# Kernel tuning notes

Measured on AMD Instinct MI355X. Metric: run time of the kernel, lower is better.

## Reference

```python
import jax, jax.numpy as jnp
import numpy as np

N_SRC = 50000
N_DST = 50000
N_EDGES = 1_600_000
D_IN = 128
D_OUT = 128
NUM_HEADS = 8
SCALE = float((D_OUT // NUM_HEADS) ** 0.5)


def setup_inputs() -> dict:
    key = jax.random.key(0)
    ks = jax.random.split(key, 10)
    s = 1.0 / np.sqrt(D_IN)
    return {
        "src_feat": jax.random.normal(ks[0], (N_SRC, D_IN), dtype=jnp.float32),
        "dst_feat": jax.random.normal(ks[1], (N_DST, D_OUT), dtype=jnp.float32),
        "src_idx": jax.random.randint(ks[2], (N_EDGES,), 0, N_SRC, dtype=jnp.int64),
        "dst_idx": jax.random.randint(ks[3], (N_EDGES,), 0, N_DST, dtype=jnp.int64),
        "Wq": jax.random.normal(ks[4], (D_OUT, D_OUT), dtype=jnp.float32) * s,
        "bq": jnp.zeros((D_OUT,), dtype=jnp.float32),
        "Wk": jax.random.normal(ks[5], (D_OUT, D_IN), dtype=jnp.float32) * s,
        "bk": jnp.zeros((D_OUT,), dtype=jnp.float32),
        "Wv": jax.random.normal(ks[6], (D_OUT, D_IN), dtype=jnp.float32) * s,
        "bv": jnp.zeros((D_OUT,), dtype=jnp.float32),
    }


def reference(src_feat, dst_feat, src_idx, dst_idx, Wq, bq, Wk, bk, Wv, bv):
    # Node-level projections (torch Linear: x @ W.T + b)
    Q = dst_feat @ Wq.T + bq            # [N_dst, D_OUT]
    K = src_feat @ Wk.T + bk            # [N_src, D_OUT]
    V = src_feat @ Wv.T + bv            # [N_src, D_OUT]

    # Edge-wise full-dim dot-product score (heads only affect the scale)
    score = jnp.sum(Q[dst_idx] * K[src_idx], axis=-1) / SCALE  # [E]

    # Segment softmax over incoming edges of each destination node
    m = jax.ops.segment_max(score, dst_idx, num_segments=N_DST)   # [N_dst]
    e = jnp.exp(score - m[dst_idx])                               # [E]
    denom = jax.ops.segment_sum(e, dst_idx, num_segments=N_DST)   # [N_dst]
    attn = e / denom[dst_idx]                                     # [E]

    # Weighted V scatter-sum to destination nodes
    out = jax.ops.segment_sum(attn[:, None] * V[src_idx], dst_idx,
                              num_segments=N_DST)                 # [N_dst, D_OUT]
    return out
```

## Files before the change

kernel.cpp:

```cpp
#include <hip/hip_runtime.h>
#include <hip/hip_bf16.h>


#define D 128
#define E1 4096
#define BCAP 10240
#define LOG2E 1.44269504088896340736f

typedef __attribute__((ext_vector_type(8))) short bf16x8;
typedef __attribute__((ext_vector_type(4))) float f32x4;
typedef __attribute__((ext_vector_type(4))) int v4i;
typedef __attribute__((ext_vector_type(4))) unsigned v4u;

static __device__ __forceinline__ unsigned short f2bf(float f) {
  unsigned u = __float_as_uint(f);
  u += 0x7fff + ((u >> 16) & 1);
  return (unsigned short)(u >> 16);
}
static __device__ __forceinline__ float bfl(unsigned u) {
  return __uint_as_float(u << 16);
}
static __device__ __forceinline__ float bfh(unsigned u) {
  return __uint_as_float(u & 0xffff0000u);
}

template <int CTRL>
static __device__ __forceinline__ float dpp_add(float x) {
  int y = __builtin_amdgcn_update_dpp(0, __float_as_int(x), CTRL, 0xF, 0xF, false);
  return x + __int_as_float(y);
}

static __device__ __forceinline__ float dot8(const float4& qa, const float4& qb,
                                             const v4u k0, const v4u k1) {
  return (qa.x * bfl(k0.x) + qa.y * bfh(k0.x) + qa.z * bfl(k0.y) +
          qa.w * bfh(k0.y)) +
         (qb.x * bfl(k1.x) + qb.y * bfh(k1.x) + qb.z * bfl(k1.y) +
          qb.w * bfh(k1.y));
}


static __device__ __forceinline__ void cvt_w_body(
    int bx, const float* __restrict__ Wq, const float* __restrict__ Wk,
    const float* __restrict__ Wv, unsigned short* __restrict__ oq,
    unsigned short* __restrict__ ok, unsigned short* __restrict__ ov, int n) {
  int i = bx * 256 + threadIdx.x;
  if (i < n) {
    oq[i] = f2bf(Wq[i]);
    ok[i] = f2bf(Wk[i]);
    ov[i] = f2bf(Wv[i]);
  }
}

static __device__ void bin1_body(
    int bx, int* h, int* basebuf, int* cur, const int* __restrict__ src_idx,
    const int* __restrict__ dst_idx, int* __restrict__ bins,
    int* __restrict__ bcount, int n) {
  const int tid = threadIdx.x;
  const int e0 = bx * E1;
  int dv[16], sv[16];
#pragma unroll
  for (int i = 0; i < 4; ++i) {
    int e = e0 + i * 1024 + tid * 4;
    if (e + 3 < n) {
      v4i d4 = __builtin_nontemporal_load((const v4i*)(dst_idx + e));
      v4i s4 = __builtin_nontemporal_load((const v4i*)(src_idx + e));
      dv[4 * i + 0] = d4.x; dv[4 * i + 1] = d4.y;
      dv[4 * i + 2] = d4.z; dv[4 * i + 3] = d4.w;
      sv[4 * i + 0] = s4.x; sv[4 * i + 1] = s4.y;
      sv[4 * i + 2] = s4.z; sv[4 * i + 3] = s4.w;
    } else {
      for (int k = 0; k < 4; ++k) {
        int ee = e + k;
        dv[4 * i + k] = (ee < n) ? dst_idx[ee] : -1;
        sv[4 * i + k] = (ee < n) ? src_idx[ee] : 0;
      }
    }
  }
  h[tid] = 0;
  __syncthreads();
#pragma unroll
  for (int i = 0; i < 16; ++i)
    if (dv[i] >= 0) atomicAdd(&h[dv[i] >> 8], 1);
  __syncthreads();
  const int c = h[tid];
  if (c > 0) basebuf[tid] = tid * BCAP + atomicAdd(&bcount[tid], c);
  cur[tid] = 0;
  __syncthreads();
#pragma unroll
  for (int i = 0; i < 16; ++i) {
    if (dv[i] >= 0) {
      const int b = dv[i] >> 8;
      const int r = atomicAdd(&cur[b], 1);
      const int off = basebuf[b] + r;
      if (off < (b + 1) * BCAP)
        bins[off] = sv[i] | ((dv[i] & 255) << 17);
    }
  }
}

static __device__ void bin2_body(
    int b, int* smem, const int* __restrict__ bins,
    const int* __restrict__ bcount, int* __restrict__ csr,
    int* __restrict__ rowptr, int n_dst, int n_edges) {
  int* h = smem;
  int* ofs = smem + 256;
  int* cur = smem + 512;
  int* red = smem + 768;
  const int tid = threadIdx.x;
  red[tid] = (tid < b) ? min(bcount[tid], BCAP) : 0;
  __syncthreads();
  for (int off = 128; off > 0; off >>= 1) {
    if (tid < off) red[tid] += red[tid + off];
    __syncthreads();
  }
  const int gbase = red[0];
  const int cnt = min(bcount[b], BCAP);
  h[tid] = 0;
  __syncthreads();
  const int* bb = bins + b * BCAP;
  for (int i = tid; i < cnt; i += 256) atomicAdd(&h[(bb[i] >> 17) & 255], 1);
  __syncthreads();
  const int myh = h[tid];
  red[tid] = myh;
  __syncthreads();
  for (int off = 1; off < 256; off <<= 1) {
    int t = (tid >= off) ? red[tid - off] : 0;
    __syncthreads();
    red[tid] += t;
    __syncthreads();
  }
  ofs[tid] = red[tid] - myh;
  cur[tid] = 0;
  const int d = b * 256 + tid;
  if (d < n_dst) rowptr[d] = gbase + ofs[tid];
  if (b == 0 && tid == 0) rowptr[n_dst] = n_edges;
  __syncthreads();
  for (int i = tid; i < cnt; i += 256) {
    const int p = bb[i];
    const int j = (p >> 17) & 255;
    const int r = atomicAdd(&cur[j], 1);
    csr[gbase + ofs[j] + r] = p & 0x1ffff;
  }
}

static __device__ void gemm_q_body(
    int bx, const float* __restrict__ X, const unsigned short* __restrict__ Wb,
    const float* __restrict__ bias, float* __restrict__ out, int N) {
  const int lane = threadIdx.x & 63;
  const int l15 = lane & 15, quad = lane >> 4;
  const int row0 = bx * 64 + (threadIdx.x >> 6) * 16;

  f32x4 acc[8];
#pragma unroll
  for (int t = 0; t < 8; ++t) acc[t] = (f32x4){0.f, 0.f, 0.f, 0.f};

  int ar = row0 + l15;
  if (ar >= N) ar = N - 1;
  const float* ap = X + (size_t)ar * D + quad * 8;

#pragma unroll
  for (int kc = 0; kc < 4; ++kc) {
    float4 a0 = *(const float4*)(ap + kc * 32);
    float4 a1 = *(const float4*)(ap + kc * 32 + 4);
    bf16x8 a;
    a[0] = f2bf(a0.x); a[1] = f2bf(a0.y); a[2] = f2bf(a0.z); a[3] = f2bf(a0.w);
    a[4] = f2bf(a1.x); a[5] = f2bf(a1.y); a[6] = f2bf(a1.z); a[7] = f2bf(a1.w);
#pragma unroll
    for (int t = 0; t < 8; ++t) {
      bf16x8 b =
          *(const bf16x8*)(Wb + (size_t)(t * 16 + l15) * D + kc * 32 + quad * 8);
      acc[t] = __builtin_amdgcn_mfma_f32_16x16x32_bf16(a, b, acc[t], 0, 0, 0);
    }
  }
#pragma unroll
  for (int t = 0; t < 8; ++t) {
    const int c = t * 16 + l15;
    const float bc = bias[c];
#pragma unroll
    for (int r = 0; r < 4; ++r) {
      const int row = row0 + quad * 4 + r;
      if (row < N) out[(size_t)row * D + c] = acc[t][r] + bc;
    }
  }
}

static __device__ void gemm_kv_body(
    int bx, unsigned short (*stage)[256], const float* __restrict__ X,
    const unsigned short* __restrict__ Wk, const float* __restrict__ bk,
    const unsigned short* __restrict__ Wv, const float* __restrict__ bv,
    unsigned short* __restrict__ KV, int N) {
  const int tid = threadIdx.x;
  const int lane = tid & 63;
  const int l15 = lane & 15, quad = lane >> 4;
  const int wave = tid >> 6;
  const int row0 = bx * 64 + wave * 16;

  f32x4 accK[8], accV[8];
#pragma unroll
  for (int t = 0; t < 8; ++t) {
    accK[t] = (f32x4){0.f, 0.f, 0.f, 0.f};
    accV[t] = (f32x4){0.f, 0.f, 0.f, 0.f};
  }

  int ar = row0 + l15;
  if (ar >= N) ar = N - 1;
  const float* ap = X + (size_t)ar * D + quad * 8;

#pragma unroll
  for (int kc = 0; kc < 4; ++kc) {
    float4 a0 = *(const float4*)(ap + kc * 32);
    float4 a1 = *(const float4*)(ap + kc * 32 + 4);
    bf16x8 a;
    a[0] = f2bf(a0.x); a[1] = f2bf(a0.y); a[2] = f2bf(a0.z); a[3] = f2bf(a0.w);
    a[4] = f2bf(a1.x); a[5] = f2bf(a1.y); a[6] = f2bf(a1.z); a[7] = f2bf(a1.w);
#pragma unroll
    for (int t = 0; t < 8; ++t) {
      const size_t boff = (size_t)(t * 16 + l15) * D + kc * 32 + quad * 8;
      bf16x8 b0 = *(const bf16x8*)(Wk + boff);
      bf16x8 b1 = *(const bf16x8*)(Wv + boff);
      accK[t] = __builtin_amdgcn_mfma_f32_16x16x32_bf16(a, b0, accK[t], 0, 0, 0);
      accV[t] = __builtin_amdgcn_mfma_f32_16x16x32_bf16(a, b1, accV[t], 0, 0, 0);
    }
  }
#pragma unroll
  for (int t = 0; t < 8; ++t) {
    const int c = t * 16 + l15;
    const float bkc = bk[c], bvc = bv[c];
    const int ki = ((c >> 2) << 3) + (c & 3);
#pragma unroll
    for (int r = 0; r < 4; ++r) {
      const int lr = wave * 16 + quad * 4 + r;
      stage[lr][ki] = f2bf(accK[t][r] + bkc);
      stage[lr][ki + 4] = f2bf(accV[t][r] + bvc);
    }
  }
  __syncthreads();
  const int row_base = bx * 64;
#pragma unroll
  for (int i = 0; i < 8; ++i) {
    int idx = i * 256 + tid;
    int lr = idx >> 5;
    int c8 = (idx & 31) << 3;
    int grow = row_base + lr;
    if (grow < N)
      *(f32x4*)(KV + (size_t)grow * 256 + c8) = *(const f32x4*)&stage[lr][c8];
  }
}


__global__ __launch_bounds__(256) void front_kernel(
    const float* __restrict__ Wq, const float* __restrict__ Wk,
    const float* __restrict__ Wv, unsigned short* __restrict__ oq,
    unsigned short* __restrict__ ok, unsigned short* __restrict__ ov, int nw,
    const int* __restrict__ src_idx, const int* __restrict__ dst_idx,
    int* __restrict__ bins, int* __restrict__ bcount, int n_edges, int gcvt) {
  __shared__ int sh[768];
  const int b = blockIdx.x;
  if (b < gcvt) {
    cvt_w_body(b, Wq, Wk, Wv, oq, ok, ov, nw);
  } else {
    bin1_body(b - gcvt, sh, sh + 256, sh + 512, src_idx, dst_idx, bins, bcount,
              n_edges);
  }
}

__global__ __launch_bounds__(256) void mid_kernel(
    const float* __restrict__ dst_feat, const unsigned short* __restrict__ Wqb,
    const float* __restrict__ bq, float* __restrict__ Q, int n_dst,
    const float* __restrict__ src_feat, const unsigned short* __restrict__ Wkb,
    const float* __restrict__ bk, const unsigned short* __restrict__ Wvb,
    const float* __restrict__ bv, unsigned short* __restrict__ KV, int n_src,
    const int* __restrict__ bins, const int* __restrict__ bcount,
    int* __restrict__ csr, int* __restrict__ rowptr, int n_edges, int nbk,
    int gq) {
  __shared__ unsigned short stage[64][256];
  const int b = blockIdx.x;
  if (b < nbk) {
    bin2_body(b, (int*)stage, bins, bcount, csr, rowptr, n_dst, n_edges);
  } else if (b < nbk + gq) {
    gemm_q_body(b - nbk, dst_feat, Wqb, bq, Q, n_dst);
  } else {
    gemm_kv_body(b - nbk - gq, stage, src_feat, Wkb, bk, Wvb, bv, KV, n_src);
  }
}

__global__ __launch_bounds__(256) void fused_agg_kernel(
    const float* __restrict__ Q, const unsigned short* __restrict__ KV,
    const int* __restrict__ csr, const int* __restrict__ rowptr,
    float* __restrict__ out, int n_dst) {
  const int lane = threadIdx.x & 63;
  const int g = lane >> 4;
  const int gl = lane & 15;
  const int stride = gridDim.x * 4;
  const float qs = 0.25f * LOG2E;

  for (int dd = blockIdx.x * 4 + (threadIdx.x >> 6); dd < n_dst; dd += stride) {
    const int d = __builtin_amdgcn_readfirstlane(dd);
    const int start = __builtin_amdgcn_readfirstlane(rowptr[d]);
    const int n = __builtin_amdgcn_readfirstlane(rowptr[d + 1]) - start;

    float4 q0 = *(const float4*)(Q + (size_t)d * D + 4 * gl);
    float4 q1 = *(const float4*)(Q + (size_t)d * D + 64 + 4 * gl);
    q0.x *= qs; q0.y *= qs; q0.z *= qs; q0.w *= qs;
    q1.x *= qs; q1.y *= qs; q1.z *= qs; q1.w *= qs;

    f32x4 acc0 = (f32x4){0.f, 0.f, 0.f, 0.f};
    f32x4 acc1 = (f32x4){0.f, 0.f, 0.f, 0.f};
    float den = 0.f;
    const int* cp = csr + start;

    for (int base = 0; base < n; base += 64) {
      const int il = base + lane;
      const int iv = __builtin_nontemporal_load(cp + ((il < n) ? il : (n - 1)));
      const int m = min(64, n - base);
      for (int j = 0; j < m; j += 16) {
        const int s0 = __shfl(iv, j + g, 64);
        const int s1 = __shfl(iv, j + 4 + g, 64);
        const int s2 = __shfl(iv, j + 8 + g, 64);
        const int s3 = __shfl(iv, j + 12 + g, 64);
        const unsigned short* r0 = KV + (size_t)s0 * 256 + gl * 8;
        const unsigned short* r1 = KV + (size_t)s1 * 256 + gl * 8;
        const unsigned short* r2 = KV + (size_t)s2 * 256 + gl * 8;
        const unsigned short* r3 = KV + (size_t)s3 * 256 + gl * 8;
        const v4u a0 = *(const v4u*)(r0);
        const v4u a1 = *(const v4u*)(r0 + 128);
        const v4u b0 = *(const v4u*)(r1);
        const v4u b1 = *(const v4u*)(r1 + 128);
        const v4u c0 = *(const v4u*)(r2);
        const v4u c1 = *(const v4u*)(r2 + 128);
        const v4u e0 = *(const v4u*)(r3);
        const v4u e1 = *(const v4u*)(r3 + 128);

        float p0 = dot8(q0, q1, a0, a1);
        float p1 = dot8(q0, q1, b0, b1);
        float p2 = dot8(q0, q1, c0, c1);
        float p3 = dot8(q0, q1, e0, e1);

        p0 = dpp_add<0xB1>(p0);  p1 = dpp_add<0xB1>(p1);
        p2 = dpp_add<0xB1>(p2);  p3 = dpp_add<0xB1>(p3);
        p0 = dpp_add<0x4E>(p0);  p1 = dpp_add<0x4E>(p1);
        p2 = dpp_add<0x4E>(p2);  p3 = dpp_add<0x4E>(p3);
        p0 = dpp_add<0x141>(p0); p1 = dpp_add<0x141>(p1);
        p2 = dpp_add<0x141>(p2); p3 = dpp_add<0x141>(p3);
        p0 = dpp_add<0x140>(p0); p1 = dpp_add<0x140>(p1);
        p2 = dpp_add<0x140>(p2); p3 = dpp_add<0x140>(p3);

        const float w0 = (j + g < m)      ? exp2f(p0) : 0.f;
        const float w1 = (j + 4 + g < m)  ? exp2f(p1) : 0.f;
        const float w2 = (j + 8 + g < m)  ? exp2f(p2) : 0.f;
        const float w3 = (j + 12 + g < m) ? exp2f(p3) : 0.f;

        acc0[0] += w0 * bfl(a0.z) + w1 * bfl(b0.z) + w2 * bfl(c0.z) + w3 * bfl(e0.z);
        acc0[1] += w0 * bfh(a0.z) + w1 * bfh(b0.z) + w2 * bfh(c0.z) + w3 * bfh(e0.z);
        acc0[2] += w0 * bfl(a0.w) + w1 * bfl(b0.w) + w2 * bfl(c0.w) + w3 * bfl(e0.w);
        acc0[3] += w0 * bfh(a0.w) + w1 * bfh(b0.w) + w2 * bfh(c0.w) + w3 * bfh(e0.w);
        acc1[0] += w0 * bfl(a1.z) + w1 * bfl(b1.z) + w2 * bfl(c1.z) + w3 * bfl(e1.z);
        acc1[1] += w0 * bfh(a1.z) + w1 * bfh(b1.z) + w2 * bfh(c1.z) + w3 * bfh(e1.z);
        acc1[2] += w0 * bfl(a1.w) + w1 * bfl(b1.w) + w2 * bfl(c1.w) + w3 * bfl(e1.w);
        acc1[3] += w0 * bfh(a1.w) + w1 * bfh(b1.w) + w2 * bfh(c1.w) + w3 * bfh(e1.w);
        den += (w0 + w1) + (w2 + w3);
      }
    }

#pragma unroll
    for (int msk = 16; msk <= 32; msk <<= 1) {
      acc0[0] += __shfl_xor(acc0[0], msk, 64);
      acc0[1] += __shfl_xor(acc0[1], msk, 64);
      acc0[2] += __shfl_xor(acc0[2], msk, 64);
      acc0[3] += __shfl_xor(acc0[3], msk, 64);
      acc1[0] += __shfl_xor(acc1[0], msk, 64);
      acc1[1] += __shfl_xor(acc1[1], msk, 64);
      acc1[2] += __shfl_xor(acc1[2], msk, 64);
      acc1[3] += __shfl_xor(acc1[3], msk, 64);
      den += __shfl_xor(den, msk, 64);
    }

    if (lane < 16) {
      const float r = (n > 0) ? 1.0f / den : 0.f;
      f32x4 o0 = (f32x4){acc0[0] * r, acc0[1] * r, acc0[2] * r, acc0[3] * r};
      f32x4 o1 = (f32x4){acc1[0] * r, acc1[1] * r, acc1[2] * r, acc1[3] * r};
      __builtin_nontemporal_store(o0, (f32x4*)(out + (size_t)d * D + 4 * gl));
      __builtin_nontemporal_store(o1,
                                  (f32x4*)(out + (size_t)d * D + 64 + 4 * gl));
    }
  }
}

extern "C" void kernel_launch(void* const* d_in, const int* in_sizes, int n_in,
                              void* d_out, int out_size, void* d_ws,
                              size_t ws_size, hipStream_t stream) {
  const float* src_feat = (const float*)d_in[0];
  const float* dst_feat = (const float*)d_in[1];
  const int* src_idx = (const int*)d_in[2];
  const int* dst_idx = (const int*)d_in[3];
  const float* Wq = (const float*)d_in[4];
  const float* bq = (const float*)d_in[5];
  const float* Wk = (const float*)d_in[6];
  const float* bk = (const float*)d_in[7];
  const float* Wv = (const float*)d_in[8];
  const float* bv = (const float*)d_in[9];

  const int n_src = in_sizes[0] / D;
  const int n_dst = in_sizes[1] / D;
  const int n_edges = in_sizes[2];
  const int nbk = (n_dst + 255) >> 8;

  float* out = (float*)d_out;

  float* Q = (float*)d_ws;
  unsigned short* KV = (unsigned short*)(Q + (size_t)n_dst * D);
  unsigned short* Wqb = KV + (size_t)n_src * 256;
  unsigned short* Wkb = Wqb + D * D;
  unsigned short* Wvb = Wkb + D * D;
  int* bcount = (int*)(Wvb + D * D);
  int* rowptr = bcount + 256;
  int* csr = rowptr + (n_dst + 1);
  int* bins = csr + n_edges;

  (void)hipMemsetAsync(bcount, 0, 256 * sizeof(int), stream);

  dim3 blk(256);
  const int gcvt = (D * D + 255) / 256;
  const int g1 = (n_edges + E1 - 1) / E1;
  const int gq = (n_dst + 63) / 64;
  const int gkv = (n_src + 63) / 64;

  front_kernel<<<dim3(gcvt + g1), blk, 0, stream>>>(
      Wq, Wk, Wv, Wqb, Wkb, Wvb, D * D, src_idx, dst_idx, bins, bcount,
      n_edges, gcvt);

  mid_kernel<<<dim3(nbk + gq + gkv), blk, 0, stream>>>(
      dst_feat, Wqb, bq, Q, n_dst, src_feat, Wkb, bk, Wvb, bv, KV, n_src, bins,
      bcount, csr, rowptr, n_edges, nbk, gq);

  int gfa = (n_dst + 3) / 4;
  if (gfa > 2048) gfa = 2048;
  fused_agg_kernel<<<dim3(gfa), blk, 0, stream>>>(Q, KV, csr, rowptr, out,
                                                  n_dst);
}
```

Measured before the change: 291.0 us.

## Inline weight bf16 conversion into GEMMs and split aggregation into three launches

Removes the separate weight-conversion blocks and their workspace buffers, so the GEMMs now load fp32 weights and convert them to bf16 in registers. This drops a dependency stage but adds conversion work inside every GEMM tile. The aggregation kernel no longer uses a grid-stride loop and launches one block per four destinations, split across three identical kernels with offset indices. The extra launches add overhead, and any benefit from the split is unclear.

```diff
diff --git a/kernel.cpp b/kernel.cpp
--- a/kernel.cpp
+++ b/kernel.cpp
@@ -38,17 +38,14 @@
           qb.w * bfh(k1.y));
 }
 
-
-static __device__ __forceinline__ void cvt_w_body(
-    int bx, const float* __restrict__ Wq, const float* __restrict__ Wk,
-    const float* __restrict__ Wv, unsigned short* __restrict__ oq,
-    unsigned short* __restrict__ ok, unsigned short* __restrict__ ov, int n) {
-  int i = bx * 256 + threadIdx.x;
-  if (i < n) {
-    oq[i] = f2bf(Wq[i]);
-    ok[i] = f2bf(Wk[i]);
-    ov[i] = f2bf(Wv[i]);
-  }
+static __device__ __forceinline__ bf16x8 ldw(const float* __restrict__ W,
+                                             size_t off) {
+  float4 w0 = *(const float4*)(W + off);
+  float4 w1 = *(const float4*)(W + off + 4);
+  bf16x8 b;
+  b[0] = f2bf(w0.x); b[1] = f2bf(w0.y); b[2] = f2bf(w0.z); b[3] = f2bf(w0.w);
+  b[4] = f2bf(w1.x); b[5] = f2bf(w1.y); b[6] = f2bf(w1.z); b[7] = f2bf(w1.w);
+  return b;
 }
 
 static __device__ void bin1_body(
@@ -144,7 +141,7 @@
 }
 
 static __device__ void gemm_q_body(
-    int bx, const float* __restrict__ X, const unsigned short* __restrict__ Wb,
+    int bx, const float* __restrict__ X, const float* __restrict__ Wf,
     const float* __restrict__ bias, float* __restrict__ out, int N) {
   const int lane = threadIdx.x & 63;
   const int l15 = lane & 15, quad = lane >> 4;
@@ -167,8 +164,7 @@
     a[4] = f2bf(a1.x); a[5] = f2bf(a1.y); a[6] = f2bf(a1.z); a[7] = f2bf(a1.w);
 #pragma unroll
     for (int t = 0; t < 8; ++t) {
-      bf16x8 b =
-          *(const bf16x8*)(Wb + (size_t)(t * 16 + l15) * D + kc * 32 + quad * 8);
+      bf16x8 b = ldw(Wf, (size_t)(t * 16 + l15) * D + kc * 32 + quad * 8);
       acc[t] = __builtin_amdgcn_mfma_f32_16x16x32_bf16(a, b, acc[t], 0, 0, 0);
     }
   }
@@ -186,8 +182,8 @@
 
 static __device__ void gemm_kv_body(
     int bx, unsigned short (*stage)[256], const float* __restrict__ X,
-    const unsigned short* __restrict__ Wk, const float* __restrict__ bk,
-    const unsigned short* __restrict__ Wv, const float* __restrict__ bv,
+    const float* __restrict__ Wkf, const float* __restrict__ bk,
+    const float* __restrict__ Wvf, const float* __restrict__ bv,
     unsigned short* __restrict__ KV, int N) {
   const int tid = threadIdx.x;
   const int lane = tid & 63;
@@ -216,8 +212,8 @@
 #pragma unroll
     for (int t = 0; t < 8; ++t) {
       const size_t boff = (size_t)(t * 16 + l15) * D + kc * 32 + quad * 8;
-      bf16x8 b0 = *(const bf16x8*)(Wk + boff);
-      bf16x8 b1 = *(const bf16x8*)(Wv + boff);
+      bf16x8 b0 = ldw(Wkf, boff);
+      bf16x8 b1 = ldw(Wvf, boff);
       accK[t] = __builtin_amdgcn_mfma_f32_16x16x32_bf16(a, b0, accK[t], 0, 0, 0);
       accV[t] = __builtin_amdgcn_mfma_f32_16x16x32_bf16(a, b1, accV[t], 0, 0, 0);
     }
@@ -247,28 +243,120 @@
   }
 }
 
+static __device__ void fused_body(
+    int v, const float* __restrict__ Q, const unsigned short* __restrict__ KV,
+    const int* __restrict__ csr, const int* __restrict__ rowptr,
+    float* __restrict__ out, int n_dst) {
+  const int lane = threadIdx.x & 63;
+  const int g = lane >> 4;
+  const int gl = lane & 15;
+  int d = v * 4 + (threadIdx.x >> 6);
+  if (d >= n_dst) return;
+  d = __builtin_amdgcn_readfirstlane(d);
+  const int start = __builtin_amdgcn_readfirstlane(rowptr[d]);
+  const int n = __builtin_amdgcn_readfirstlane(rowptr[d + 1]) - start;
+
+  const float qs = 0.25f * LOG2E;
+  float4 q0 = *(const float4*)(Q + (size_t)d * D + 4 * gl);
+  float4 q1 = *(const float4*)(Q + (size_t)d * D + 64 + 4 * gl);
+  q0.x *= qs; q0.y *= qs; q0.z *= qs; q0.w *= qs;
+  q1.x *= qs; q1.y *= qs; q1.z *= qs; q1.w *= qs;
+
+  f32x4 acc0 = (f32x4){0.f, 0.f, 0.f, 0.f};
+  f32x4 acc1 = (f32x4){0.f, 0.f, 0.f, 0.f};
+  float den = 0.f;
+  const int* cp = csr + start;
+
+  for (int base = 0; base < n; base += 64) {
+    const int il = base + lane;
+    const int iv = __builtin_nontemporal_load(cp + ((il < n) ? il : (n - 1)));
+    const int m = min(64, n - base);
+    for (int j = 0; j < m; j += 16) {
+      const int s0 = __shfl(iv, j + g, 64);
+      const int s1 = __shfl(iv, j + 4 + g, 64);
+      const int s2 = __shfl(iv, j + 8 + g, 64);
+      const int s3 = __shfl(iv, j + 12 + g, 64);
+      const unsigned short* r0 = KV + (size_t)s0 * 256 + gl * 8;
+      const unsigned short* r1 = KV + (size_t)s1 * 256 + gl * 8;
+      const unsigned short* r2 = KV + (size_t)s2 * 256 + gl * 8;
+      const unsigned short* r3 = KV + (size_t)s3 * 256 + gl * 8;
+      const v4u a0 = *(const v4u*)(r0);
+      const v4u a1 = *(const v4u*)(r0 + 128);
+      const v4u b0 = *(const v4u*)(r1);
+      const v4u b1 = *(const v4u*)(r1 + 128);
+      const v4u c0 = *(const v4u*)(r2);
+      const v4u c1 = *(const v4u*)(r2 + 128);
+      const v4u e0 = *(const v4u*)(r3);
+      const v4u e1 = *(const v4u*)(r3 + 128);
+
+      float p0 = dot8(q0, q1, a0, a1);
+      float p1 = dot8(q0, q1, b0, b1);
+      float p2 = dot8(q0, q1, c0, c1);
+      float p3 = dot8(q0, q1, e0, e1);
+
+      p0 = dpp_add<0xB1>(p0);  p1 = dpp_add<0xB1>(p1);
+      p2 = dpp_add<0xB1>(p2);  p3 = dpp_add<0xB1>(p3);
+      p0 = dpp_add<0x4E>(p0);  p1 = dpp_add<0x4E>(p1);
+      p2 = dpp_add<0x4E>(p2);  p3 = dpp_add<0x4E>(p3);
+      p0 = dpp_add<0x141>(p0); p1 = dpp_add<0x141>(p1);
+      p2 = dpp_add<0x141>(p2); p3 = dpp_add<0x141>(p3);
+      p0 = dpp_add<0x140>(p0); p1 = dpp_add<0x140>(p1);
+      p2 = dpp_add<0x140>(p2); p3 = dpp_add<0x140>(p3);
+
+      const float w0 = (j + g < m)      ? exp2f(p0) : 0.f;
+      const float w1 = (j + 4 + g < m)  ? exp2f(p1) : 0.f;
+      const float w2 = (j + 8 + g < m)  ? exp2f(p2) : 0.f;
+      const float w3 = (j + 12 + g < m) ? exp2f(p3) : 0.f;
+
+      acc0[0] += w0 * bfl(a0.z) + w1 * bfl(b0.z) + w2 * bfl(c0.z) + w3 * bfl(e0.z);
+      acc0[1] += w0 * bfh(a0.z) + w1 * bfh(b0.z) + w2 * bfh(c0.z) + w3 * bfh(e0.z);
+      acc0[2] += w0 * bfl(a0.w) + w1 * bfl(b0.w) + w2 * bfl(c0.w) + w3 * bfl(e0.w);
+      acc0[3] += w0 * bfh(a0.w) + w1 * bfh(b0.w) + w2 * bfh(c0.w) + w3 * bfh(e0.w);
+      acc1[0] += w0 * bfl(a1.z) + w1 * bfl(b1.z) + w2 * bfl(c1.z) + w3 * bfl(e1.z);
+      acc1[1] += w0 * bfh(a1.z) + w1 * bfh(b1.z) + w2 * bfh(c1.z) + w3 * bfh(e1.z);
+      acc1[2] += w0 * bfl(a1.w) + w1 * bfl(b1.w) + w2 * bfl(c1.w) + w3 * bfl(e1.w);
+      acc1[3] += w0 * bfh(a1.w) + w1 * bfh(b1.w) + w2 * bfh(c1.w) + w3 * bfh(e1.w);
+      den += (w0 + w1) + (w2 + w3);
+    }
+  }
+
+#pragma unroll
+  for (int msk = 16; msk <= 32; msk <<= 1) {
+    acc0[0] += __shfl_xor(acc0[0], msk, 64);
+    acc0[1] += __shfl_xor(acc0[1], msk, 64);
+    acc0[2] += __shfl_xor(acc0[2], msk, 64);
+    acc0[3] += __shfl_xor(acc0[3], msk, 64);
+    acc1[0] += __shfl_xor(acc1[0], msk, 64);
+    acc1[1] += __shfl_xor(acc1[1], msk, 64);
+    acc1[2] += __shfl_xor(acc1[2], msk, 64);
+    acc1[3] += __shfl_xor(acc1[3], msk, 64);
+    den += __shfl_xor(den, msk, 64);
+  }
+
+  if (lane < 16) {
+    const float r = (n > 0) ? 1.0f / den : 0.f;
+    f32x4 o0 = (f32x4){acc0[0] * r, acc0[1] * r, acc0[2] * r, acc0[3] * r};
+    f32x4 o1 = (f32x4){acc1[0] * r, acc1[1] * r, acc1[2] * r, acc1[3] * r};
+    __builtin_nontemporal_store(o0, (f32x4*)(out + (size_t)d * D + 4 * gl));
+    __builtin_nontemporal_store(o1,
+                                (f32x4*)(out + (size_t)d * D + 64 + 4 * gl));
+  }
+}
+
 
 __global__ __launch_bounds__(256) void front_kernel(
-    const float* __restrict__ Wq, const float* __restrict__ Wk,
-    const float* __restrict__ Wv, unsigned short* __restrict__ oq,
-    unsigned short* __restrict__ ok, unsigned short* __restrict__ ov, int nw,
     const int* __restrict__ src_idx, const int* __restrict__ dst_idx,
-    int* __restrict__ bins, int* __restrict__ bcount, int n_edges, int gcvt) {
+    int* __restrict__ bins, int* __restrict__ bcount, int n_edges) {
   __shared__ int sh[768];
-  const int b = blockIdx.x;
-  if (b < gcvt) {
-    cvt_w_body(b, Wq, Wk, Wv, oq, ok, ov, nw);
-  } else {
-    bin1_body(b - gcvt, sh, sh + 256, sh + 512, src_idx, dst_idx, bins, bcount,
-              n_edges);
-  }
+  bin1_body(blockIdx.x, sh, sh + 256, sh + 512, src_idx, dst_idx, bins, bcount,
+            n_edges);
 }
 
 __global__ __launch_bounds__(256) void mid_kernel(
-    const float* __restrict__ dst_feat, const unsigned short* __restrict__ Wqb,
+    const float* __restrict__ dst_feat, const float* __restrict__ Wq,
     const float* __restrict__ bq, float* __restrict__ Q, int n_dst,
-    const float* __restrict__ src_feat, const unsigned short* __restrict__ Wkb,
-    const float* __restrict__ bk, const unsigned short* __restrict__ Wvb,
+    const float* __restrict__ src_feat, const float* __restrict__ Wk,
+    const float* __restrict__ bk, const float* __restrict__ Wv,
     const float* __restrict__ bv, unsigned short* __restrict__ KV, int n_src,
     const int* __restrict__ bins, const int* __restrict__ bcount,
     int* __restrict__ csr, int* __restrict__ rowptr, int n_edges, int nbk,
@@ -278,112 +366,29 @@
   if (b < nbk) {
     bin2_body(b, (int*)stage, bins, bcount, csr, rowptr, n_dst, n_edges);
   } else if (b < nbk + gq) {
-    gemm_q_body(b - nbk, dst_feat, Wqb, bq, Q, n_dst);
+    gemm_q_body(b - nbk, dst_feat, Wq, bq, Q, n_dst);
   } else {
-    gemm_kv_body(b - nbk - gq, stage, src_feat, Wkb, bk, Wvb, bv, KV, n_src);
-  }
-}
-
-__global__ __launch_bounds__(256) void fused_agg_kernel(
+    gemm_kv_body(b - nbk - gq, stage, src_feat, Wk, bk, Wv, bv, KV, n_src);
+  }
+}
+
+__global__ __launch_bounds__(256) void fused_agg_k0(
     const float* __restrict__ Q, const unsigned short* __restrict__ KV,
     const int* __restrict__ csr, const int* __restrict__ rowptr,
-    float* __restrict__ out, int n_dst) {
-  const int lane = threadIdx.x & 63;
-  const int g = lane >> 4;
-  const int gl = lane & 15;
-  const int stride = gridDim.x * 4;
-  const float qs = 0.25f * LOG2E;
-
-  for (int dd = blockIdx.x * 4 + (threadIdx.x >> 6); dd < n_dst; dd += stride) {
-    const int d = __builtin_amdgcn_readfirstlane(dd);
-    const int start = __builtin_amdgcn_readfirstlane(rowptr[d]);
-    const int n = __builtin_amdgcn_readfirstlane(rowptr[d + 1]) - start;
-
-    float4 q0 = *(const float4*)(Q + (size_t)d * D + 4 * gl);
-    float4 q1 = *(const float4*)(Q + (size_t)d * D + 64 + 4 * gl);
-    q0.x *= qs; q0.y *= qs; q0.z *= qs; q0.w *= qs;
-    q1.x *= qs; q1.y *= qs; q1.z *= qs; q1.w *= qs;
-
-    f32x4 acc0 = (f32x4){0.f, 0.f, 0.f, 0.f};
-    f32x4 acc1 = (f32x4){0.f, 0.f, 0.f, 0.f};
-    float den = 0.f;
-    const int* cp = csr + start;
-
-    for (int base = 0; base < n; base += 64) {
-      const int il = base + lane;
-      const int iv = __builtin_nontemporal_load(cp + ((il < n) ? il : (n - 1)));
-      const int m = min(64, n - base);
-      for (int j = 0; j < m; j += 16) {
-        const int s0 = __shfl(iv, j + g, 64);
-        const int s1 = __shfl(iv, j + 4 + g, 64);
-        const int s2 = __shfl(iv, j + 8 + g, 64);
-        const int s3 = __shfl(iv, j + 12 + g, 64);
-        const unsigned short* r0 = KV + (size_t)s0 * 256 + gl * 8;
-        const unsigned short* r1 = KV + (size_t)s1 * 256 + gl * 8;
-        const unsigned short* r2 = KV + (size_t)s2 * 256 + gl * 8;
-        const unsigned short* r3 = KV + (size_t)s3 * 256 + gl * 8;
-        const v4u a0 = *(const v4u*)(r0);
-        const v4u a1 = *(const v4u*)(r0 + 128);
-        const v4u b0 = *(const v4u*)(r1);
-        const v4u b1 = *(const v4u*)(r1 + 128);
-        const v4u c0 = *(const v4u*)(r2);
-        const v4u c1 = *(const v4u*)(r2 + 128);
-        const v4u e0 = *(const v4u*)(r3);
-        const v4u e1 = *(const v4u*)(r3 + 128);
-
-        float p0 = dot8(q0, q1, a0, a1);
-        float p1 = dot8(q0, q1, b0, b1);
-        float p2 = dot8(q0, q1, c0, c1);
-        float p3 = dot8(q0, q1, e0, e1);
-
-        p0 = dpp_add<0xB1>(p0);  p1 = dpp_add<0xB1>(p1);
-        p2 = dpp_add<0xB1>(p2);  p3 = dpp_add<0xB1>(p3);
-        p0 = dpp_add<0x4E>(p0);  p1 = dpp_add<0x4E>(p1);
-        p2 = dpp_add<0x4E>(p2);  p3 = dpp_add<0x4E>(p3);
-        p0 = dpp_add<0x141>(p0); p1 = dpp_add<0x141>(p1);
-        p2 = dpp_add<0x141>(p2); p3 = dpp_add<0x141>(p3);
-        p0 = dpp_add<0x140>(p0); p1 = dpp_add<0x140>(p1);
-        p2 = dpp_add<0x140>(p2); p3 = dpp_add<0x140>(p3);
-
-        const float w0 = (j + g < m)      ? exp2f(p0) : 0.f;
-        const float w1 = (j + 4 + g < m)  ? exp2f(p1) : 0.f;
-        const float w2 = (j + 8 + g < m)  ? exp2f(p2) : 0.f;
-        const float w3 = (j + 12 + g < m) ? exp2f(p3) : 0.f;
-
-        acc0[0] += w0 * bfl(a0.z) + w1 * bfl(b0.z) + w2 * bfl(c0.z) + w3 * bfl(e0.z);
-        acc0[1] += w0 * bfh(a0.z) + w1 * bfh(b0.z) + w2 * bfh(c0.z) + w3 * bfh(e0.z);
-        acc0[2] += w0 * bfl(a0.w) + w1 * bfl(b0.w) + w2 * bfl(c0.w) + w3 * bfl(e0.w);
-        acc0[3] += w0 * bfh(a0.w) + w1 * bfh(b0.w) + w2 * bfh(c0.w) + w3 * bfh(e0.w);
-        acc1[0] += w0 * bfl(a1.z) + w1 * bfl(b1.z) + w2 * bfl(c1.z) + w3 * bfl(e1.z);
-        acc1[1] += w0 * bfh(a1.z) + w1 * bfh(b1.z) + w2 * bfh(c1.z) + w3 * bfh(e1.z);
-        acc1[2] += w0 * bfl(a1.w) + w1 * bfl(b1.w) + w2 * bfl(c1.w) + w3 * bfl(e1.w);
-        acc1[3] += w0 * bfh(a1.w) + w1 * bfh(b1.w) + w2 * bfh(c1.w) + w3 * bfh(e1.w);
-        den += (w0 + w1) + (w2 + w3);
-      }
-    }
-
-#pragma unroll
-    for (int msk = 16; msk <= 32; msk <<= 1) {
-      acc0[0] += __shfl_xor(acc0[0], msk, 64);
-      acc0[1] += __shfl_xor(acc0[1], msk, 64);
-      acc0[2] += __shfl_xor(acc0[2], msk, 64);
-      acc0[3] += __shfl_xor(acc0[3], msk, 64);
-      acc1[0] += __shfl_xor(acc1[0], msk, 64);
-      acc1[1] += __shfl_xor(acc1[1], msk, 64);
-      acc1[2] += __shfl_xor(acc1[2], msk, 64);
-      acc1[3] += __shfl_xor(acc1[3], msk, 64);
-      den += __shfl_xor(den, msk, 64);
-    }
-
-    if (lane < 16) {
-      const float r = (n > 0) ? 1.0f / den : 0.f;
-      f32x4 o0 = (f32x4){acc0[0] * r, acc0[1] * r, acc0[2] * r, acc0[3] * r};
-      f32x4 o1 = (f32x4){acc1[0] * r, acc1[1] * r, acc1[2] * r, acc1[3] * r};
-      __builtin_nontemporal_store(o0, (f32x4*)(out + (size_t)d * D + 4 * gl));
-      __builtin_nontemporal_store(o1,
-                                  (f32x4*)(out + (size_t)d * D + 64 + 4 * gl));
-    }
-  }
+    float* __restrict__ out, int n_dst, int voff) {
+  fused_body(blockIdx.x + voff, Q, KV, csr, rowptr, out, n_dst);
+}
+__global__ __launch_bounds__(256) void fused_agg_k1(
+    const float* __restrict__ Q, const unsigned short* __restrict__ KV,
+    const int* __restrict__ csr, const int* __restrict__ rowptr,
+    float* __restrict__ out, int n_dst, int voff) {
+  fused_body(blockIdx.x + voff, Q, KV, csr, rowptr, out, n_dst);
+}
+__global__ __launch_bounds__(256) void fused_agg_k2(
+    const float* __restrict__ Q, const unsigned short* __restrict__ KV,
+    const int* __restrict__ csr, const int* __restrict__ rowptr,
+    float* __restrict__ out, int n_dst, int voff) {
+  fused_body(blockIdx.x + voff, Q, KV, csr, rowptr, out, n_dst);
 }
 
 extern "C" void kernel_launch(void* const* d_in, const int* in_sizes, int n_in,
@@ -409,10 +414,7 @@
 
   float* Q = (float*)d_ws;
   unsigned short* KV = (unsigned short*)(Q + (size_t)n_dst * D);
-  unsigned short* Wqb = KV + (size_t)n_src * 256;
-  unsigned short* Wkb = Wqb + D * D;
-  unsigned short* Wvb = Wkb + D * D;
-  int* bcount = (int*)(Wvb + D * D);
+  int* bcount = (int*)(KV + (size_t)n_src * 256);
   int* rowptr = bcount + 256;
   int* csr = rowptr + (n_dst + 1);
   int* bins = csr + n_edges;
@@ -420,21 +422,24 @@
   (void)hipMemsetAsync(bcount, 0, 256 * sizeof(int), stream);
 
   dim3 blk(256);
-  const int gcvt = (D * D + 255) / 256;
   const int g1 = (n_edges + E1 - 1) / E1;
   const int gq = (n_dst + 63) / 64;
   const int gkv = (n_src + 63) / 64;
-
-  front_kernel<<<dim3(gcvt + g1), blk, 0, stream>>>(
-      Wq, Wk, Wv, Wqb, Wkb, Wvb, D * D, src_idx, dst_idx, bins, bcount,
-      n_edges, gcvt);
+  const int nf = (n_dst + 3) / 4;
+  const int nf3 = (nf + 2) / 3;
+
+  front_kernel<<<dim3(g1), blk, 0, stream>>>(src_idx, dst_idx, bins, bcount,
+                                             n_edges);
 
   mid_kernel<<<dim3(nbk + gq + gkv), blk, 0, stream>>>(
-      dst_feat, Wqb, bq, Q, n_dst, src_feat, Wkb, bk, Wvb, bv, KV, n_src, bins,
+      dst_feat, Wq, bq, Q, n_dst, src_feat, Wk, bk, Wv, bv, KV, n_src, bins,
       bcount, csr, rowptr, n_edges, nbk, gq);
 
-  int gfa = (n_dst + 3) / 4;
-  if (gfa > 2048) gfa = 2048;
-  fused_agg_kernel<<<dim3(gfa), blk, 0, stream>>>(Q, KV, csr, rowptr, out,
-                                                  n_dst);
-}
+  const int v0 = 0, v1 = nf3, v2 = 2 * nf3;
+  fused_agg_k0<<<dim3(nf3), blk, 0, stream>>>(Q, KV, csr, rowptr, out, n_dst,
+                                              v0);
+  fused_agg_k1<<<dim3(nf3), blk, 0, stream>>>(Q, KV, csr, rowptr, out, n_dst,
+                                              v1);
+  fused_agg_k2<<<dim3(nf - v2), blk, 0, stream>>>(Q, KV, csr, rowptr, out,
+                                                  n_dst, v2);
+}
```

New measurement: 341.6 us. 17.4% more time.
